# Kernel optimization log

Measured on AMD Instinct MI355X. Metric: run time of the kernel, lower is better.

The kernel has to match this reference:

```python
import jax, jax.numpy as jnp
import numpy as np
import math

B, E, H, HD, P, G, N, L, FF = 16, 768, 12, 64, 16, 14, 196, 12, 3072
SQRT_E = math.sqrt(E)
SQRT_HD = math.sqrt(HD)


def cosine_norm(x):
    n = jnp.linalg.norm(x, axis=-1, keepdims=True)
    return x / jnp.maximum(n, 1e-6)


def layer_norm(x, w, b, eps=1e-6):
    m = jnp.mean(x, axis=-1, keepdims=True)
    v = jnp.var(x, axis=-1, keepdims=True)
    return (x - m) / jnp.sqrt(v + eps) * w + b


def setup_inputs() -> dict:
    key = jax.random.key(0)
    ks = jax.random.split(key, 16)
    std = 0.02
    return {
        "x": jax.random.normal(ks[0], (B, 3, 224, 224), jnp.float32),
        "patch_w": jax.random.normal(ks[1], (E, 3, P, P), jnp.float32) * std,
        "patch_b": jnp.zeros((E,), jnp.float32),
        "cls_token": jax.random.normal(ks[2], (1, 1, E), jnp.float32) * std,
        "pos_embed": jax.random.normal(ks[3], (1, N + 1, E), jnp.float32) * std,
        "Wq": jax.random.normal(ks[4], (L, E, E), jnp.float32) * std,
        "Wk": jax.random.normal(ks[5], (L, E, E), jnp.float32) * std,
        "Wv": jax.random.normal(ks[6], (L, E, E), jnp.float32) * std,
        "Wo": jax.random.normal(ks[7], (L, E, E), jnp.float32) * std,
        # Scale params stored at their torch init values (s = ones * scale)
        "s_qk": jnp.ones((L, H, HD), jnp.float32) / SQRT_E,        # scale=1/sqrt(dim)
        "Wup": jax.random.normal(ks[8], (L, FF, E), jnp.float32) * std,
        "Wgate": jax.random.normal(ks[9], (L, FF, E), jnp.float32) * std,
        "Wdown": jax.random.normal(ks[10], (L, E, FF), jnp.float32) * std,
        "s_u": jnp.ones((L, FF), jnp.float32),
        "s_v": jnp.ones((L, FF), jnp.float32),
        "alpha_A": jnp.ones((L, E), jnp.float32) / SQRT_E,         # scale=1/sqrt(dim)
        "alpha_M": jnp.ones((L, E), jnp.float32) / SQRT_E,
        "fc_w": jnp.ones((E,), jnp.float32),
        "fc_b": jnp.zeros((E,), jnp.float32),
    }


def _attention(h, wq, wk, wv, wo, s_qk):
    b, n, _ = h.shape
    q = (h @ wq.T).reshape(b, n, H, HD)
    k = (h @ wk.T).reshape(b, n, H, HD)
    v = (h @ wv.T).reshape(b, n, H, HD)
    # Scale.forward(): s * (init/scale) with init=1, scale=1/sqrt(E)
    s = s_qk * SQRT_E                                   # [H, HD]
    q = cosine_norm(q) * s
    k = cosine_norm(k) * s
    logits = jnp.einsum("bnhd,bmhd->bhnm", q, k) * SQRT_HD
    attn = jax.nn.softmax(logits, axis=-1)
    out = jnp.einsum("bhnm,bmhd->bnhd", attn, v).reshape(b, n, E)
    return out @ wo.T


def _mlp(h, wup, wgate, wdown, s_u, s_v):
    u = (h @ wup.T) * s_u
    v = (h @ wgate.T) * s_v * SQRT_E                    # mlp scale = sqrt(in_features)
    hidden = u * jax.nn.silu(v)
    return hidden @ wdown.T


def _block(h, wq, wk, wv, wo, s_qk, wup, wgate, wdown, s_u, s_v, a_A, a_M):
    # alpha Scale: init=0.05, scale=1/sqrt(E) -> effective = s * 0.05 * sqrt(E)
    aA = a_A * (0.05 * SQRT_E)
    aM = a_M * (0.05 * SQRT_E)
    h_A = cosine_norm(_attention(h, wq, wk, wv, wo, s_qk))
    h = cosine_norm(h + aA * (h_A - h))
    h_M = cosine_norm(_mlp(h, wup, wgate, wdown, s_u, s_v))
    h = cosine_norm(h + aM * (h_M - h))
    return h


def reference(x, patch_w, patch_b, cls_token, pos_embed, Wq, Wk, Wv, Wo, s_qk,
              Wup, Wgate, Wdown, s_u, s_v, alpha_A, alpha_M, fc_w, fc_b):
    b = x.shape[0]
    # patch embed: conv k=stride=16 == patch extraction + linear proj
    patches = x.reshape(b, 3, G, P, G, P).transpose(0, 2, 4, 1, 3, 5).reshape(b, N, 3 * P * P)
    t = patches @ patch_w.reshape(E, -1).T + patch_b    # [B, N, E]
    t = jnp.concatenate([jnp.broadcast_to(cls_token, (b, 1, E)), t], axis=1)
    t = t + pos_embed                                    # [B, N+1, E]
    nodes = None
    for i in range(L):
        t = _block(t, Wq[i], Wk[i], Wv[i], Wo[i], s_qk[i],
                   Wup[i], Wgate[i], Wdown[i], s_u[i], s_v[i], alpha_A[i], alpha_M[i])
        if i == L - 2:
            nodes = layer_norm(t, fc_w, fc_b)[:, 1:]
    edges = layer_norm(t, fc_w, fc_b)[:, 1:]
    return nodes, edges
```

## Files before the change

### kernel.cpp

```cpp
#include <hip/hip_runtime.h>
#include <hip/hip_bf16.h>
#include <cstdint>
#include <cstddef>

typedef __hip_bfloat16 bf16;
typedef short bf16x8 __attribute__((ext_vector_type(8)));
typedef float f32x4 __attribute__((ext_vector_type(4)));

#define SQRT_E   27.712812921102035f
#define ASCALE   (0.05f * 27.712812921102035f)
#define MPAD     3200

__device__ __forceinline__ void load_lds16(const bf16* g, bf16* l) {
    __builtin_amdgcn_global_load_lds(
        (const __attribute__((address_space(1))) void*)g,
        (__attribute__((address_space(3))) void*)l, 16, 0, 0);
}

__device__ __forceinline__ float block_sum(float v, float* sbuf) {
#pragma unroll
    for (int m = 32; m >= 1; m >>= 1) v += __shfl_xor(v, m);
    __syncthreads();
    if ((threadIdx.x & 63) == 0) sbuf[threadIdx.x >> 6] = v;
    __syncthreads();
    return sbuf[0] + sbuf[1] + sbuf[2] + sbuf[3];
}

__device__ __forceinline__ void cvt8(const float* s, bf16* d) {
    float4 f0 = *(const float4*)s;
    float4 f1 = *(const float4*)(s + 4);
    bf16 t[8];
    t[0] = __float2bfloat16(f0.x); t[1] = __float2bfloat16(f0.y);
    t[2] = __float2bfloat16(f0.z); t[3] = __float2bfloat16(f0.w);
    t[4] = __float2bfloat16(f1.x); t[5] = __float2bfloat16(f1.y);
    t[6] = __float2bfloat16(f1.z); t[7] = __float2bfloat16(f1.w);
    *reinterpret_cast<uint4*>(d) = *reinterpret_cast<const uint4*>(t);
}

__global__ __launch_bounds__(256) void conv1_kernel(const float* __restrict__ src,
                                                    bf16* __restrict__ dst, int n8) {
    int idx = blockIdx.x * 256 + threadIdx.x;
    if (idx >= n8) return;
    cvt8(src + (size_t)idx * 8, dst + (size_t)idx * 8);
}

__global__ __launch_bounds__(256) void wconv_kernel(
    const float* __restrict__ wq, const float* __restrict__ wk,
    const float* __restrict__ wv, const float* __restrict__ wo,
    const float* __restrict__ wu, const float* __restrict__ wg,
    const float* __restrict__ wd, bf16* __restrict__ dst) {
    int idx = blockIdx.x * 256 + threadIdx.x;
    if (idx >= 1179648) return;
    const float* src;
    size_t off;
    if (idx < 294912) {
        int seg = idx / 73728, o = idx - seg * 73728;
        src = (seg == 0) ? wq : (seg == 1) ? wk : (seg == 2) ? wv : wo;
        off = (size_t)o * 8;
    } else {
        int i2 = idx - 294912;
        int seg = i2 / 294912, o = i2 - seg * 294912;
        src = (seg == 0) ? wu : (seg == 1) ? wg : wd;
        off = (size_t)o * 8;
    }
    cvt8(src + off, dst + (size_t)idx * 8);
}

__global__ __launch_bounds__(256) void im2col_kernel(const float* __restrict__ x,
                                                     bf16* __restrict__ A) {
    int idx = blockIdx.x * 256 + threadIdx.x;
    int row = idx / 768, col = idx - row * 768;
    if (row >= 3136) { A[idx] = __float2bfloat16(0.f); return; }
    int b = row / 196, pp = row - b * 196;
    int gy = pp / 14, gx = pp - gy * 14;
    int c = col >> 8, rem = col & 255, py = rem >> 4, px = rem & 15;
    A[idx] = __float2bfloat16(
        x[((size_t)(b * 3 + c) * 224 + gy * 16 + py) * 224 + gx * 16 + px]);
}

__global__ __launch_bounds__(256) void assemble_kernel(
    const float* __restrict__ tproj, const float* __restrict__ pb,
    const float* __restrict__ cls, const float* __restrict__ pos,
    float* __restrict__ h, bf16* __restrict__ hb) {
    int row = blockIdx.x;
    int b = row / 197, n = row - b * 197;
#pragma unroll
    for (int i = 0; i < 3; i++) {
        int c = threadIdx.x + i * 256;
        float v;
        if (n == 0) v = cls[c] + pos[c];
        else v = tproj[(size_t)(b * 196 + n - 1) * 768 + c] + pb[c] + pos[(size_t)n * 768 + c];
        h[(size_t)row * 768 + c] = v;
        hb[(size_t)row * 768 + c] = __float2bfloat16(v);
    }
}

__global__ __launch_bounds__(256) void gemm_bt(
    const bf16* __restrict__ A, int lda,
    const bf16* __restrict__ B0, const bf16* __restrict__ B1, const bf16* __restrict__ B2,
    int tilesPerSeg, int segColStride,
    void* __restrict__ Cv, int ldc, long long partStride,
    int Klen, int ldb, int outBf16) {
    __shared__ __align__(16) bf16 As[128 * 32];
    __shared__ __align__(16) bf16 Bs[128 * 32];
    const int tid = threadIdx.x;
    const int lane = tid & 63, wave = tid >> 6;
    const int wm = wave & 1, wn = wave >> 1;
    const int quad = lane >> 4, l16 = lane & 15;
    const int seg = blockIdx.x / tilesPerSeg;
    const int nt = blockIdx.x - seg * tilesPerSeg;
    const bf16* B = (seg == 0) ? B0 : (seg == 1 ? B1 : B2);
    const int row0 = blockIdx.y * 128;
    const int col0 = nt * 128;
    const long long kofs = (long long)blockIdx.z * Klen;
    const bf16* Ab = A + (size_t)row0 * lda + kofs;
    const bf16* Bb = B + (size_t)col0 * ldb + kofs;
    const long long cofs = (long long)blockIdx.z * partStride + (long long)seg * segColStride;

    f32x4 acc[4][4];
    f32x4 zero = {0.f, 0.f, 0.f, 0.f};
#pragma unroll
    for (int i = 0; i < 4; i++)
#pragma unroll
        for (int j = 0; j < 4; j++) acc[i][j] = zero;

    for (int k0 = 0; k0 < Klen; k0 += 32) {
#pragma unroll
        for (int it = 0; it < 2; ++it) {
            int cidx = it * 256 + tid;
            int r = cidx >> 2, cg = cidx & 3;
            load_lds16(Ab + (size_t)r * lda + k0 + cg * 8, As + cidx * 8);
            load_lds16(Bb + (size_t)r * ldb + k0 + cg * 8, Bs + cidx * 8);
        }
        __syncthreads();
        bf16x8 av[4], bv[4];
#pragma unroll
        for (int i = 0; i < 4; i++) {
            av[i] = *(const bf16x8*)(As + (wm * 64 + i * 16 + l16) * 32 + quad * 8);
            bv[i] = *(const bf16x8*)(Bs + (wn * 64 + i * 16 + l16) * 32 + quad * 8);
        }
#pragma unroll
        for (int i = 0; i < 4; i++)
#pragma unroll
            for (int j = 0; j < 4; j++)
                acc[i][j] = __builtin_amdgcn_mfma_f32_16x16x32_bf16(av[i], bv[j], acc[i][j], 0, 0, 0);
        __syncthreads();
    }
    if (outBf16) {
        bf16* Cb = (bf16*)Cv + cofs;
#pragma unroll
        for (int i = 0; i < 4; i++) {
            int rr = row0 + wm * 64 + i * 16 + quad * 4;
#pragma unroll
            for (int j = 0; j < 4; j++) {
                int cc = col0 + wn * 64 + j * 16 + l16;
#pragma unroll
                for (int r = 0; r < 4; r++)
                    Cb[(size_t)(rr + r) * ldc + cc] = __float2bfloat16(acc[i][j][r]);
            }
        }
    } else {
        float* Cb = (float*)Cv + cofs;
#pragma unroll
        for (int i = 0; i < 4; i++) {
            int rr = row0 + wm * 64 + i * 16 + quad * 4;
#pragma unroll
            for (int j = 0; j < 4; j++) {
                int cc = col0 + wn * 64 + j * 16 + l16;
#pragma unroll
                for (int r = 0; r < 4; r++)
                    Cb[(size_t)(rr + r) * ldc + cc] = acc[i][j][r];
            }
        }
    }
}

__global__ __launch_bounds__(256) void gemm_upgate(
    const bf16* __restrict__ A, const bf16* __restrict__ Bu, const bf16* __restrict__ Bv,
    const float* __restrict__ su, const float* __restrict__ sv,
    bf16* __restrict__ H) {
    __shared__ __align__(16) bf16 As[128 * 32];
    __shared__ __align__(16) bf16 Bus[64 * 32];
    __shared__ __align__(16) bf16 Bvs[64 * 32];
    const int tid = threadIdx.x;
    const int lane = tid & 63, wave = tid >> 6;
    const int wm = wave & 1, wn = wave >> 1;
    const int quad = lane >> 4, l16 = lane & 15;
    const int ct = blockIdx.x;
    const int row0 = blockIdx.y * 128;
    const bf16* Ab = A + (size_t)row0 * 768;
    const bf16* Bub = Bu + (size_t)ct * 64 * 768;
    const bf16* Bvb = Bv + (size_t)ct * 64 * 768;

    f32x4 au[4][2], av_[4][2];
    f32x4 zero = {0.f, 0.f, 0.f, 0.f};
#pragma unroll
    for (int i = 0; i < 4; i++)
#pragma unroll
        for (int j = 0; j < 2; j++) { au[i][j] = zero; av_[i][j] = zero; }

    for (int k0 = 0; k0 < 768; k0 += 32) {
#pragma unroll
        for (int it = 0; it < 2; ++it) {
            int cidx = it * 256 + tid;
            int r = cidx >> 2, cg = cidx & 3;
            load_lds16(Ab + (size_t)r * 768 + k0 + cg * 8, As + cidx * 8);
        }
        {
            int r = tid >> 2, cg = tid & 3;
            load_lds16(Bub + (size_t)r * 768 + k0 + cg * 8, Bus + tid * 8);
            load_lds16(Bvb + (size_t)r * 768 + k0 + cg * 8, Bvs + tid * 8);
        }
        __syncthreads();
        bf16x8 a[4], bu[2], bv[2];
#pragma unroll
        for (int i = 0; i < 4; i++)
            a[i] = *(const bf16x8*)(As + (wm * 64 + i * 16 + l16) * 32 + quad * 8);
#pragma unroll
        for (int j = 0; j < 2; j++) {
            bu[j] = *(const bf16x8*)(Bus + (wn * 32 + j * 16 + l16) * 32 + quad * 8);
            bv[j] = *(const bf16x8*)(Bvs + (wn * 32 + j * 16 + l16) * 32 + quad * 8);
        }
#pragma unroll
        for (int i = 0; i < 4; i++)
#pragma unroll
            for (int j = 0; j < 2; j++) {
                au[i][j]  = __builtin_amdgcn_mfma_f32_16x16x32_bf16(a[i], bu[j], au[i][j], 0, 0, 0);
                av_[i][j] = __builtin_amdgcn_mfma_f32_16x16x32_bf16(a[i], bv[j], av_[i][j], 0, 0, 0);
            }
        __syncthreads();
    }
#pragma unroll
    for (int j = 0; j < 2; j++) {
        int cc = ct * 64 + wn * 32 + j * 16 + l16;
        float suc = su[cc];
        float svc = sv[cc] * SQRT_E;
#pragma unroll
        for (int i = 0; i < 4; i++) {
            int rr = row0 + wm * 64 + i * 16 + quad * 4;
#pragma unroll
            for (int r = 0; r < 4; r++) {
                float u = au[i][j][r] * suc;
                float v = av_[i][j][r] * svc;
                float sig = 1.f / (1.f + __expf(-v));
                H[(size_t)(rr + r) * 3072 + cc] = __float2bfloat16(u * v * sig);
            }
        }
    }
}

__global__ __launch_bounds__(256) void qk_norm_kernel(
    const bf16* __restrict__ qkv, const float* __restrict__ s_l,
    bf16* __restrict__ Q, bf16* __restrict__ K, bf16* __restrict__ VT) {
    int gw = blockIdx.x * 4 + (threadIdx.x >> 6);
    int lane = threadIdx.x & 63;
    int h = gw % 12;
    int n = (gw / 12) % 224;
    int b = gw / (12 * 224);
    int bh = b * 12 + h;
    bf16 z = __float2bfloat16(0.f);
    if (n >= 208) { VT[((size_t)bh * 64 + lane) * 224 + n] = z; return; }
    if (n >= 197) {
        Q[((size_t)bh * 208 + n) * 64 + lane] = z;
        K[((size_t)bh * 208 + n) * 64 + lane] = z;
        VT[((size_t)bh * 64 + lane) * 224 + n] = z;
        return;
    }
    size_t row = (size_t)(b * 197 + n) * 2304;
    float q = __bfloat162float(qkv[row + h * 64 + lane]);
    float k = __bfloat162float(qkv[row + 768 + h * 64 + lane]);
    float v = __bfloat162float(qkv[row + 1536 + h * 64 + lane]);
    float qs = q * q, ks = k * k;
#pragma unroll
    for (int m = 32; m >= 1; m >>= 1) { qs += __shfl_xor(qs, m); ks += __shfl_xor(ks, m); }
    float s = s_l[h * 64 + lane] * SQRT_E;
    float qn = q / fmaxf(sqrtf(qs), 1e-6f) * s;
    float kn = k / fmaxf(sqrtf(ks), 1e-6f) * s;
    Q[((size_t)bh * 208 + n) * 64 + lane] = __float2bfloat16(qn);
    K[((size_t)bh * 208 + n) * 64 + lane] = __float2bfloat16(kn);
    VT[((size_t)bh * 64 + lane) * 224 + n] = __float2bfloat16(v);
}

__global__ __launch_bounds__(64) void attn_kernel(
    const bf16* __restrict__ Q, const bf16* __restrict__ K,
    const bf16* __restrict__ VT, bf16* __restrict__ O) {
    __shared__ __align__(16) bf16 Ps[16 * 224];
    int lane = threadIdx.x;
    int quad = lane >> 4, l16 = lane & 15;
    int bh = blockIdx.x % 192;
    int qt = blockIdx.x / 192;
    int b = bh / 12, h = bh - b * 12;
    const bf16* Qb = Q + (size_t)bh * 208 * 64;
    const bf16* Kb = K + (size_t)bh * 208 * 64;
    const bf16* Vb = VT + (size_t)bh * 64 * 224;
    f32x4 zero = {0.f, 0.f, 0.f, 0.f};

    bf16x8 a0 = *(const bf16x8*)(Qb + (qt * 16 + l16) * 64 + quad * 8);
    bf16x8 a1 = *(const bf16x8*)(Qb + (qt * 16 + l16) * 64 + quad * 8 + 32);

    f32x4 lg[13];
#pragma unroll
    for (int kt = 0; kt < 13; kt++) {
        bf16x8 b0 = *(const bf16x8*)(Kb + (kt * 16 + l16) * 64 + quad * 8);
        bf16x8 b1 = *(const bf16x8*)(Kb + (kt * 16 + l16) * 64 + quad * 8 + 32);
        f32x4 c = zero;
        c = __builtin_amdgcn_mfma_f32_16x16x32_bf16(a0, b0, c, 0, 0, 0);
        c = __builtin_amdgcn_mfma_f32_16x16x32_bf16(a1, b1, c, 0, 0, 0);
        lg[kt] = c;
    }
    float mx[4] = {-3e38f, -3e38f, -3e38f, -3e38f};
#pragma unroll
    for (int kt = 0; kt < 13; kt++) {
        bool valid = (kt * 16 + l16) < 197;
#pragma unroll
        for (int r = 0; r < 4; r++) {
            float v = valid ? lg[kt][r] * 8.0f : -3e38f;
            lg[kt][r] = v;
            mx[r] = fmaxf(mx[r], v);
        }
    }
#pragma unroll
    for (int m = 1; m < 16; m <<= 1)
#pragma unroll
        for (int r = 0; r < 4; r++) mx[r] = fmaxf(mx[r], __shfl_xor(mx[r], m));
    float sm[4] = {0.f, 0.f, 0.f, 0.f};
#pragma unroll
    for (int kt = 0; kt < 13; kt++)
#pragma unroll
        for (int r = 0; r < 4; r++) {
            float p = __expf(lg[kt][r] - mx[r]);
            lg[kt][r] = p;
            sm[r] += p;
        }
#pragma unroll
    for (int m = 1; m < 16; m <<= 1)
#pragma unroll
        for (int r = 0; r < 4; r++) sm[r] += __shfl_xor(sm[r], m);
    float inv[4];
#pragma unroll
    for (int r = 0; r < 4; r++) inv[r] = 1.f / sm[r];
#pragma unroll
    for (int kt = 0; kt < 13; kt++)
#pragma unroll
        for (int r = 0; r < 4; r++)
            Ps[(quad * 4 + r) * 224 + kt * 16 + l16] = __float2bfloat16(lg[kt][r] * inv[r]);
#pragma unroll
    for (int r = 0; r < 4; r++)
        Ps[(quad * 4 + r) * 224 + 208 + l16] = __float2bfloat16(0.f);
    __syncthreads();
#pragma unroll
    for (int nt = 0; nt < 4; nt++) {
        f32x4 o = zero;
#pragma unroll
        for (int ks = 0; ks < 7; ks++) {
            bf16x8 pa = *(const bf16x8*)(Ps + l16 * 224 + ks * 32 + quad * 8);
            bf16x8 vb = *(const bf16x8*)(Vb + (nt * 16 + l16) * 224 + ks * 32 + quad * 8);
            o = __builtin_amdgcn_mfma_f32_16x16x32_bf16(pa, vb, o, 0, 0, 0);
        }
#pragma unroll
        for (int r = 0; r < 4; r++) {
            int tok = qt * 16 + quad * 4 + r;
            if (tok < 197)
                O[(size_t)(b * 197 + tok) * 768 + h * 64 + nt * 16 + l16] = __float2bfloat16(o[r]);
        }
    }
}

__global__ __launch_bounds__(256) void residual_cos(
    const float* __restrict__ proj, int nParts, long long partStride,
    const float* __restrict__ alpha,
    float* __restrict__ h, bf16* __restrict__ hb) {
    __shared__ float sbuf[4];
    int row = blockIdx.x, tid = threadIdx.x;
    float p[3];
    float ss = 0.f;
#pragma unroll
    for (int i = 0; i < 3; i++) {
        int c = tid + i * 256;
        float v = 0.f;
        for (int pt = 0; pt < nParts; pt++) v += proj[(long long)pt * partStride + (size_t)row * 768 + c];
        p[i] = v;
        ss += v * v;
    }
    ss = block_sum(ss, sbuf);
    float inv1 = 1.f / fmaxf(sqrtf(ss), 1e-6f);
    float ss2 = 0.f;
#pragma unroll
    for (int i = 0; i < 3; i++) {
        int c = tid + i * 256;
        float hv = h[(size_t)row * 768 + c];
        float a = alpha[c] * ASCALE;
        float m = hv + a * (p[i] * inv1 - hv);
        p[i] = m;
        ss2 += m * m;
    }
    ss2 = block_sum(ss2, sbuf);
    float inv2 = 1.f / fmaxf(sqrtf(ss2), 1e-6f);
#pragma unroll
    for (int i = 0; i < 3; i++) {
        int c = tid + i * 256;
        float v = p[i] * inv2;
        h[(size_t)row * 768 + c] = v;
        hb[(size_t)row * 768 + c] = __float2bfloat16(v);
    }
}

__global__ __launch_bounds__(256) void layernorm_out(
    const float* __restrict__ h, const float* __restrict__ w,
    const float* __restrict__ bia, float* __restrict__ out) {
    __shared__ float sbuf[4];
    int bi = blockIdx.x;
    int b = bi / 196, j = bi - b * 196;
    int row = b * 197 + j + 1;
    int tid = threadIdx.x;
    float xv[3];
    float s = 0.f;
#pragma unroll
    for (int i = 0; i < 3; i++) {
        xv[i] = h[(size_t)row * 768 + tid + i * 256];
        s += xv[i];
    }
    s = block_sum(s, sbuf);
    float mean = s * (1.f / 768.f);
    float s2 = 0.f;
#pragma unroll
    for (int i = 0; i < 3; i++) { float d = xv[i] - mean; s2 += d * d; }
    s2 = block_sum(s2, sbuf);
    float var = s2 * (1.f / 768.f);
    float invs = 1.f / sqrtf(var + 1e-6f);
#pragma unroll
    for (int i = 0; i < 3; i++) {
        int c = tid + i * 256;
        out[(size_t)bi * 768 + c] = (xv[i] - mean) * invs * w[c] + bia[c];
    }
}

extern "C" void kernel_launch(void* const* d_in, const int* in_sizes, int n_in,
                              void* d_out, int out_size, void* d_ws, size_t ws_size,
                              hipStream_t stream) {
    (void)in_sizes; (void)n_in; (void)out_size; (void)ws_size;
    const float* x      = (const float*)d_in[0];
    const float* patchw = (const float*)d_in[1];
    const float* patchb = (const float*)d_in[2];
    const float* cls    = (const float*)d_in[3];
    const float* pos    = (const float*)d_in[4];
    const float* Wq     = (const float*)d_in[5];
    const float* Wk     = (const float*)d_in[6];
    const float* Wv     = (const float*)d_in[7];
    const float* Wo     = (const float*)d_in[8];
    const float* s_qk   = (const float*)d_in[9];
    const float* Wup    = (const float*)d_in[10];
    const float* Wgate  = (const float*)d_in[11];
    const float* Wdown  = (const float*)d_in[12];
    const float* s_u    = (const float*)d_in[13];
    const float* s_v    = (const float*)d_in[14];
    const float* alA    = (const float*)d_in[15];
    const float* alM    = (const float*)d_in[16];
    const float* fcw    = (const float*)d_in[17];
    const float* fcb    = (const float*)d_in[18];
    float* out = (float*)d_out;

    char* ws = (char*)d_ws;
    size_t ofs = 0;
    auto alloc = [&](size_t bytes) -> void* {
        void* p = ws + ofs;
        ofs += (bytes + 255) & ~(size_t)255;
        return p;
    };
    float* h      = (float*)alloc((size_t)MPAD * 768 * 4);
    float* part   = (float*)alloc((size_t)4 * MPAD * 768 * 4);
    bf16*  qkvb   = (bf16*)alloc((size_t)MPAD * 2304 * 2);
    bf16*  hb     = (bf16*)alloc((size_t)MPAD * 768 * 2);
    bf16*  attno  = (bf16*)alloc((size_t)MPAD * 768 * 2);
    bf16*  hidden = (bf16*)alloc((size_t)MPAD * 3072 * 2);
    bf16*  wbf    = (bf16*)alloc((size_t)9437184 * 2);

    float* tproj  = part;
    bf16*  Qb     = (bf16*)part;
    bf16*  Kb     = Qb + (size_t)192 * 208 * 64;
    bf16*  VTb    = Kb + (size_t)192 * 208 * 64;
    bf16*  Apatch = hidden;

    bf16* wqb = wbf;
    bf16* wkb = wbf + 589824;
    bf16* wvb = wbf + 1179648;
    bf16* wob = wbf + 1769472;
    bf16* wub = wbf + 2359296;
    bf16* wgb = wbf + 4718592;
    bf16* wdb = wbf + 7077888;

    const long long PSTR = (long long)MPAD * 768;
    const size_t EE = 768 * 768, FE = (size_t)3072 * 768;

    conv1_kernel<<<288, 256, 0, stream>>>(patchw, wqb, 73728);
    im2col_kernel<<<9600, 256, 0, stream>>>(x, Apatch);
    gemm_bt<<<dim3(6, 25, 1), 256, 0, stream>>>(Apatch, 768, wqb, wqb, wqb,
                                                6, 0, tproj, 768, 0, 768, 768, 0);
    assemble_kernel<<<3152, 256, 0, stream>>>(tproj, patchb, cls, pos, h, hb);

    for (int l = 0; l < 12; l++) {
        wconv_kernel<<<4608, 256, 0, stream>>>(Wq + (size_t)l * EE, Wk + (size_t)l * EE,
                                               Wv + (size_t)l * EE, Wo + (size_t)l * EE,
                                               Wup + (size_t)l * FE, Wgate + (size_t)l * FE,
                                               Wdown + (size_t)l * FE, wbf);
        gemm_bt<<<dim3(18, 25, 1), 256, 0, stream>>>(hb, 768, wqb, wkb, wvb,
                                                     6, 768, qkvb, 2304, 0, 768, 768, 1);
        qk_norm_kernel<<<10752, 256, 0, stream>>>(qkvb, s_qk + (size_t)l * 768, Qb, Kb, VTb);
        attn_kernel<<<2496, 64, 0, stream>>>(Qb, Kb, VTb, attno);
        gemm_bt<<<dim3(6, 25, 2), 256, 0, stream>>>(attno, 768, wob, wob, wob,
                                                    6, 0, part, 768, PSTR, 384, 768, 0);
        residual_cos<<<3152, 256, 0, stream>>>(part, 2, PSTR, alA + (size_t)l * 768, h, hb);
        gemm_upgate<<<dim3(48, 25), 256, 0, stream>>>(hb, wub, wgb,
                                                      s_u + (size_t)l * 3072,
                                                      s_v + (size_t)l * 3072, hidden);
        gemm_bt<<<dim3(6, 25, 4), 256, 0, stream>>>(hidden, 3072, wdb, wdb, wdb,
                                                    6, 0, part, 768, PSTR, 768, 3072, 0);
        residual_cos<<<3152, 256, 0, stream>>>(part, 4, PSTR, alM + (size_t)l * 768, h, hb);

        if (l == 10) layernorm_out<<<3136, 256, 0, stream>>>(h, fcw, fcb, out);
        if (l == 11) layernorm_out<<<3136, 256, 0, stream>>>(h, fcw, fcb, out + 2408448);
    }
}
```

Before: 2.617 ms.

## Double GEMM K-tile to 64 with XOR-swizzled LDS and batch all-layer weight conversion

Both GEMM kernels now stage a 64-wide K slice per iteration instead of 32, with an XOR swizzle on the 16-byte column chunk so the LDS fragment reads avoid bank conflicts. This halves the barrier count per K and doubles the MFMA work between syncs. Separately, when the workspace is large enough, all 12 layers' weights are converted to bf16 in one launch up front instead of one launch per layer. The costs are doubled LDS per block, which may reduce occupancy, and a much larger workspace footprint.

```diff
diff --git a/kernel.cpp b/kernel.cpp
--- a/kernel.cpp
+++ b/kernel.cpp
@@ -66,6 +66,30 @@
     cvt8(src + off, dst + (size_t)idx * 8);
 }
 
+__global__ __launch_bounds__(256) void wconv_all_kernel(
+    const float* __restrict__ wq, const float* __restrict__ wk,
+    const float* __restrict__ wv, const float* __restrict__ wo,
+    const float* __restrict__ wu, const float* __restrict__ wg,
+    const float* __restrict__ wd, bf16* __restrict__ dst) {
+    int idx = blockIdx.x * 256 + threadIdx.x;
+    int l = idx / 1179648;
+    int o = idx - l * 1179648;
+    const float* src;
+    size_t off;
+    if (o < 294912) {
+        int seg = o / 73728, oo = o - seg * 73728;
+        src = ((seg == 0) ? wq : (seg == 1) ? wk : (seg == 2) ? wv : wo)
+              + (size_t)l * 589824;
+        off = (size_t)oo * 8;
+    } else {
+        int i2 = o - 294912;
+        int seg = i2 / 294912, oo = i2 - seg * 294912;
+        src = ((seg == 0) ? wu : (seg == 1) ? wg : wd) + (size_t)l * 2359296;
+        off = (size_t)oo * 8;
+    }
+    cvt8(src + off, dst + (size_t)idx * 8);
+}
+
 __global__ __launch_bounds__(256) void im2col_kernel(const float* __restrict__ x,
                                                      bf16* __restrict__ A) {
     int idx = blockIdx.x * 256 + threadIdx.x;
@@ -101,12 +125,13 @@
     int tilesPerSeg, int segColStride,
     void* __restrict__ Cv, int ldc, long long partStride,
     int Klen, int ldb, int outBf16) {
-    __shared__ __align__(16) bf16 As[128 * 32];
-    __shared__ __align__(16) bf16 Bs[128 * 32];
+    __shared__ __align__(16) bf16 As[128 * 64];
+    __shared__ __align__(16) bf16 Bs[128 * 64];
     const int tid = threadIdx.x;
     const int lane = tid & 63, wave = tid >> 6;
     const int wm = wave & 1, wn = wave >> 1;
     const int quad = lane >> 4, l16 = lane & 15;
+    const int rsw = l16 & 7;
     const int seg = blockIdx.x / tilesPerSeg;
     const int nt = blockIdx.x - seg * tilesPerSeg;
     const bf16* B = (seg == 0) ? B0 : (seg == 1 ? B1 : B2);
@@ -124,26 +149,31 @@
 #pragma unroll
         for (int j = 0; j < 4; j++) acc[i][j] = zero;
 
-    for (int k0 = 0; k0 < Klen; k0 += 32) {
-#pragma unroll
-        for (int it = 0; it < 2; ++it) {
+    for (int k0 = 0; k0 < Klen; k0 += 64) {
+#pragma unroll
+        for (int it = 0; it < 4; ++it) {
             int cidx = it * 256 + tid;
-            int r = cidx >> 2, cg = cidx & 3;
-            load_lds16(Ab + (size_t)r * lda + k0 + cg * 8, As + cidx * 8);
-            load_lds16(Bb + (size_t)r * ldb + k0 + cg * 8, Bs + cidx * 8);
+            int r = cidx >> 3, cg = cidx & 7;
+            int cs = cg ^ (r & 7);
+            load_lds16(Ab + (size_t)r * lda + k0 + cs * 8, As + cidx * 8);
+            load_lds16(Bb + (size_t)r * ldb + k0 + cs * 8, Bs + cidx * 8);
         }
         __syncthreads();
-        bf16x8 av[4], bv[4];
-#pragma unroll
-        for (int i = 0; i < 4; i++) {
-            av[i] = *(const bf16x8*)(As + (wm * 64 + i * 16 + l16) * 32 + quad * 8);
-            bv[i] = *(const bf16x8*)(Bs + (wn * 64 + i * 16 + l16) * 32 + quad * 8);
-        }
-#pragma unroll
-        for (int i = 0; i < 4; i++)
-#pragma unroll
-            for (int j = 0; j < 4; j++)
-                acc[i][j] = __builtin_amdgcn_mfma_f32_16x16x32_bf16(av[i], bv[j], acc[i][j], 0, 0, 0);
+#pragma unroll
+        for (int ks = 0; ks < 2; ks++) {
+            bf16x8 av[4], bv[4];
+            const int ch = (ks * 4 + quad);
+#pragma unroll
+            for (int i = 0; i < 4; i++) {
+                av[i] = *(const bf16x8*)(As + (wm * 64 + i * 16 + l16) * 64 + (ch ^ rsw) * 8);
+                bv[i] = *(const bf16x8*)(Bs + (wn * 64 + i * 16 + l16) * 64 + (ch ^ rsw) * 8);
+            }
+#pragma unroll
+            for (int i = 0; i < 4; i++)
+#pragma unroll
+                for (int j = 0; j < 4; j++)
+                    acc[i][j] = __builtin_amdgcn_mfma_f32_16x16x32_bf16(av[i], bv[j], acc[i][j], 0, 0, 0);
+        }
         __syncthreads();
     }
     if (outBf16) {
@@ -179,13 +209,14 @@
     const bf16* __restrict__ A, const bf16* __restrict__ Bu, const bf16* __restrict__ Bv,
     const float* __restrict__ su, const float* __restrict__ sv,
     bf16* __restrict__ H) {
-    __shared__ __align__(16) bf16 As[128 * 32];
-    __shared__ __align__(16) bf16 Bus[64 * 32];
-    __shared__ __align__(16) bf16 Bvs[64 * 32];
+    __shared__ __align__(16) bf16 As[128 * 64];
+    __shared__ __align__(16) bf16 Bus[64 * 64];
+    __shared__ __align__(16) bf16 Bvs[64 * 64];
     const int tid = threadIdx.x;
     const int lane = tid & 63, wave = tid >> 6;
     const int wm = wave & 1, wn = wave >> 1;
     const int quad = lane >> 4, l16 = lane & 15;
+    const int rsw = l16 & 7;
     const int ct = blockIdx.x;
     const int row0 = blockIdx.y * 128;
     const bf16* Ab = A + (size_t)row0 * 768;
@@ -199,35 +230,43 @@
 #pragma unroll
         for (int j = 0; j < 2; j++) { au[i][j] = zero; av_[i][j] = zero; }
 
-    for (int k0 = 0; k0 < 768; k0 += 32) {
+    for (int k0 = 0; k0 < 768; k0 += 64) {
+#pragma unroll
+        for (int it = 0; it < 4; ++it) {
+            int cidx = it * 256 + tid;
+            int r = cidx >> 3, cg = cidx & 7;
+            int cs = cg ^ (r & 7);
+            load_lds16(Ab + (size_t)r * 768 + k0 + cs * 8, As + cidx * 8);
+        }
 #pragma unroll
         for (int it = 0; it < 2; ++it) {
             int cidx = it * 256 + tid;
-            int r = cidx >> 2, cg = cidx & 3;
-            load_lds16(Ab + (size_t)r * 768 + k0 + cg * 8, As + cidx * 8);
-        }
-        {
-            int r = tid >> 2, cg = tid & 3;
-            load_lds16(Bub + (size_t)r * 768 + k0 + cg * 8, Bus + tid * 8);
-            load_lds16(Bvb + (size_t)r * 768 + k0 + cg * 8, Bvs + tid * 8);
+            int r = cidx >> 3, cg = cidx & 7;
+            int cs = cg ^ (r & 7);
+            load_lds16(Bub + (size_t)r * 768 + k0 + cs * 8, Bus + cidx * 8);
+            load_lds16(Bvb + (size_t)r * 768 + k0 + cs * 8, Bvs + cidx * 8);
         }
         __syncthreads();
-        bf16x8 a[4], bu[2], bv[2];
-#pragma unroll
-        for (int i = 0; i < 4; i++)
-            a[i] = *(const bf16x8*)(As + (wm * 64 + i * 16 + l16) * 32 + quad * 8);
-#pragma unroll
-        for (int j = 0; j < 2; j++) {
-            bu[j] = *(const bf16x8*)(Bus + (wn * 32 + j * 16 + l16) * 32 + quad * 8);
-            bv[j] = *(const bf16x8*)(Bvs + (wn * 32 + j * 16 + l16) * 32 + quad * 8);
-        }
-#pragma unroll
-        for (int i = 0; i < 4; i++)
+#pragma unroll
+        for (int ks = 0; ks < 2; ks++) {
+            bf16x8 a[4], bu[2], bv[2];
+            const int ch = (ks * 4 + quad);
+#pragma unroll
+            for (int i = 0; i < 4; i++)
+                a[i] = *(const bf16x8*)(As + (wm * 64 + i * 16 + l16) * 64 + (ch ^ rsw) * 8);
 #pragma unroll
             for (int j = 0; j < 2; j++) {
-                au[i][j]  = __builtin_amdgcn_mfma_f32_16x16x32_bf16(a[i], bu[j], au[i][j], 0, 0, 0);
-                av_[i][j] = __builtin_amdgcn_mfma_f32_16x16x32_bf16(a[i], bv[j], av_[i][j], 0, 0, 0);
+                bu[j] = *(const bf16x8*)(Bus + (wn * 32 + j * 16 + l16) * 64 + (ch ^ rsw) * 8);
+                bv[j] = *(const bf16x8*)(Bvs + (wn * 32 + j * 16 + l16) * 64 + (ch ^ rsw) * 8);
             }
+#pragma unroll
+            for (int i = 0; i < 4; i++)
+#pragma unroll
+                for (int j = 0; j < 2; j++) {
+                    au[i][j]  = __builtin_amdgcn_mfma_f32_16x16x32_bf16(a[i], bu[j], au[i][j], 0, 0, 0);
+                    av_[i][j] = __builtin_amdgcn_mfma_f32_16x16x32_bf16(a[i], bv[j], av_[i][j], 0, 0, 0);
+                }
+        }
         __syncthreads();
     }
 #pragma unroll
@@ -438,7 +477,7 @@
 extern "C" void kernel_launch(void* const* d_in, const int* in_sizes, int n_in,
                               void* d_out, int out_size, void* d_ws, size_t ws_size,
                               hipStream_t stream) {
-    (void)in_sizes; (void)n_in; (void)out_size; (void)ws_size;
+    (void)in_sizes; (void)n_in; (void)out_size;
     const float* x      = (const float*)d_in[0];
     const float* patchw = (const float*)d_in[1];
     const float* patchb = (const float*)d_in[2];
@@ -473,7 +512,9 @@
     bf16*  hb     = (bf16*)alloc((size_t)MPAD * 768 * 2);
     bf16*  attno  = (bf16*)alloc((size_t)MPAD * 768 * 2);
     bf16*  hidden = (bf16*)alloc((size_t)MPAD * 3072 * 2);
-    bf16*  wbf    = (bf16*)alloc((size_t)9437184 * 2);
+    const size_t WPL = 9437184;
+    bool ALLW = (ofs + (size_t)12 * WPL * 2) <= ws_size;
+    bf16*  wbf    = (bf16*)alloc((ALLW ? (size_t)12 * WPL : WPL) * 2);
 
     float* tproj  = part;
     bf16*  Qb     = (bf16*)part;
@@ -481,28 +522,32 @@
     bf16*  VTb    = Kb + (size_t)192 * 208 * 64;
     bf16*  Apatch = hidden;
 
-    bf16* wqb = wbf;
-    bf16* wkb = wbf + 589824;
-    bf16* wvb = wbf + 1179648;
-    bf16* wob = wbf + 1769472;
-    bf16* wub = wbf + 2359296;
-    bf16* wgb = wbf + 4718592;
-    bf16* wdb = wbf + 7077888;
-
     const long long PSTR = (long long)MPAD * 768;
     const size_t EE = 768 * 768, FE = (size_t)3072 * 768;
 
-    conv1_kernel<<<288, 256, 0, stream>>>(patchw, wqb, 73728);
+    conv1_kernel<<<288, 256, 0, stream>>>(patchw, wbf, 73728);
     im2col_kernel<<<9600, 256, 0, stream>>>(x, Apatch);
-    gemm_bt<<<dim3(6, 25, 1), 256, 0, stream>>>(Apatch, 768, wqb, wqb, wqb,
+    gemm_bt<<<dim3(6, 25, 1), 256, 0, stream>>>(Apatch, 768, wbf, wbf, wbf,
                                                 6, 0, tproj, 768, 0, 768, 768, 0);
     assemble_kernel<<<3152, 256, 0, stream>>>(tproj, patchb, cls, pos, h, hb);
 
+    if (ALLW)
+        wconv_all_kernel<<<55296, 256, 0, stream>>>(Wq, Wk, Wv, Wo, Wup, Wgate, Wdown, wbf);
+
     for (int l = 0; l < 12; l++) {
-        wconv_kernel<<<4608, 256, 0, stream>>>(Wq + (size_t)l * EE, Wk + (size_t)l * EE,
-                                               Wv + (size_t)l * EE, Wo + (size_t)l * EE,
-                                               Wup + (size_t)l * FE, Wgate + (size_t)l * FE,
-                                               Wdown + (size_t)l * FE, wbf);
+        bf16* wl  = wbf + (ALLW ? (size_t)l * WPL : 0);
+        bf16* wqb = wl;
+        bf16* wkb = wl + 589824;
+        bf16* wvb = wl + 1179648;
+        bf16* wob = wl + 1769472;
+        bf16* wub = wl + 2359296;
+        bf16* wgb = wl + 4718592;
+        bf16* wdb = wl + 7077888;
+        if (!ALLW)
+            wconv_kernel<<<4608, 256, 0, stream>>>(Wq + (size_t)l * EE, Wk + (size_t)l * EE,
+                                                   Wv + (size_t)l * EE, Wo + (size_t)l * EE,
+                                                   Wup + (size_t)l * FE, Wgate + (size_t)l * FE,
+                                                   Wdown + (size_t)l * FE, wl);
         gemm_bt<<<dim3(18, 25, 1), 256, 0, stream>>>(hb, 768, wqb, wkb, wvb,
                                                      6, 768, qkvb, 2304, 0, 768, 768, 1);
         qk_norm_kernel<<<10752, 256, 0, stream>>>(qkvb, s_qk + (size_t)l * 768, Qb, Kb, VTb);
```

After: 2.688 ms. 1.03x slower.
